# Optimization experiments

Hardware: AMD Instinct MI355X
Metric: run time of the kernel (lower is better)

The kernel has to match this reference:

```python
import jax, jax.numpy as jnp
import numpy as np

B, N, IN_DIM, HID = 16, 1024, 2, 64
GDEP = 2
ALPHA = 3.0                      # DGCRM/DGCN tanh alpha
GC_ALPHA, GC_BETA, GC_GAMMA = 0.05, 0.95, 0.95  # list_weight
HYPER, MID, NODE_DIM = 32, 16, 40
CIN = HID + IN_DIM               # 66
CAT = (GDEP + 1) * CIN           # 198


def setup_inputs() -> dict:
    key = jax.random.key(0)
    ks = jax.random.split(key, 14)
    x = jax.random.normal(ks[0], (B, N, IN_DIM), jnp.float32)
    hidden_state = 0.1 * jax.random.normal(ks[1], (B, N, HID), jnp.float32)
    nodevec1 = jax.random.normal(ks[2], (N, NODE_DIM), jnp.float32)
    nodevec2 = jax.random.normal(ks[3], (N, NODE_DIM), jnp.float32)
    A0 = jax.random.uniform(ks[4], (N, N), jnp.float32)
    A0 = A0 / A0.sum(-1, keepdims=True)
    A1 = jax.random.uniform(ks[5], (N, N), jnp.float32)
    A1 = A1 / A1.sum(-1, keepdims=True)
    s = 0.05  # small init scale
    hyper_W1 = s * jax.random.normal(ks[6], (4, CAT, HYPER), jnp.float32)
    hyper_b1 = jnp.zeros((4, HYPER), jnp.float32)
    hyper_W2 = s * jax.random.normal(ks[7], (4, HYPER, MID), jnp.float32)
    hyper_b2 = jnp.zeros((4, MID), jnp.float32)
    hyper_W3 = s * jax.random.normal(ks[8], (4, MID, NODE_DIM), jnp.float32)
    hyper_b3 = jnp.zeros((4, NODE_DIM), jnp.float32)
    rnn_W = s * jax.random.normal(ks[9], (6, CAT, HID), jnp.float32)
    rnn_b = jnp.zeros((6, HID), jnp.float32)
    return dict(x=x, hidden_state=hidden_state, nodevec1=nodevec1, nodevec2=nodevec2,
                A0=A0, A1=A1, hyper_W1=hyper_W1, hyper_b1=hyper_b1,
                hyper_W2=hyper_W2, hyper_b2=hyper_b2, hyper_W3=hyper_W3,
                hyper_b3=hyper_b3, rnn_W=rnn_W, rnn_b=rnn_b)


def reference(x, hidden_state, nodevec1, nodevec2, A0, A1,
              hyper_W1, hyper_b1, hyper_W2, hyper_b2, hyper_W3, hyper_b3,
              rnn_W, rnn_b):
    def gconv_hyper(inp, adj, i):
        # K-hop diffusion: h = alpha*x + gamma * (h^T adj) over node dim
        h = inp
        outs = [h]
        for _ in range(GDEP):
            h = GC_ALPHA * inp + GC_GAMMA * jnp.einsum('bnc,nm->bmc', h, adj)
            outs.append(h)
        ho = jnp.concatenate(outs, axis=-1)           # [B,N,(gdep+1)*CIN]
        ho = jax.nn.sigmoid(ho @ hyper_W1[i] + hyper_b1[i])
        ho = jax.nn.sigmoid(ho @ hyper_W2[i] + hyper_b2[i])
        return ho @ hyper_W3[i] + hyper_b3[i]         # [B,N,NODE_DIM]

    def gconv_rnn(inp, i):
        # FAITHFUL to source bug: stray leading '+' makes the beta/gamma
        # einsum terms standalone no-op statements, so each hop is h=alpha*x.
        outs = [inp] + [GC_ALPHA * inp] * GDEP
        return jnp.concatenate(outs, axis=-1) @ rnn_W[i] + rnn_b[i]

    # --- DGCN: dynamic adjacency generation ---
    hyper_input = jnp.concatenate((x, hidden_state), axis=-1)  # [B,N,CIN]
    filter1 = gconv_hyper(hyper_input, A0, 0) + gconv_hyper(hyper_input, A1, 1)
    filter2 = gconv_hyper(hyper_input, A0, 2) + gconv_hyper(hyper_input, A1, 3)
    nv1 = jnp.tanh(ALPHA * nodevec1[None] * filter1)  # [B,N,NODE_DIM]
    nv2 = jnp.tanh(ALPHA * nodevec2[None] * filter2)
    a = jnp.einsum('bnd,bmd->bnm', nv1, nv2) - jnp.einsum('bnd,bmd->bnm', nv2, nv1)
    adp_raw = jax.nn.relu(jnp.tanh(ALPHA * a))        # [B,N,N]
    eye = jnp.eye(N, dtype=adp_raw.dtype)
    def norm(adj):
        adj = adj + eye
        return adj / adj.sum(-1, keepdims=True)
    adp = norm(adp_raw)                               # computed as in source
    adpT = norm(jnp.swapaxes(adp_raw, 1, 2))          # (unused downstream due to
    del adp, adpT                                     #  the GConv_RNN source bug)

    # --- GRU-style gating ---
    combined = jnp.concatenate((x, hidden_state), axis=-1)
    z = jax.nn.sigmoid(gconv_rnn(combined, 0) + gconv_rnn(combined, 1))
    r = jax.nn.sigmoid(gconv_rnn(combined, 2) + gconv_rnn(combined, 3))
    candidate = jnp.concatenate((x, r * hidden_state), axis=-1)
    hc = jnp.tanh(gconv_rnn(candidate, 4) + gconv_rnn(candidate, 5))
    h = z * hidden_state + (1.0 - z) * hc             # [B,N,HID]
    return h
```

## Files before the change

### kernel.cpp

```cpp
#include <hip/hip_runtime.h>
#include <math.h>

#define NTOK   16384
#define CIN_   66
#define HID_   64
#define NCH    192
#define TPB    64

__global__ void fold_weights(const float* __restrict__ rnn_W,
                             const float* __restrict__ rnn_b,
                             float* __restrict__ Wf,
                             float* __restrict__ bf)
{
    int idx = blockIdx.x * blockDim.x + threadIdx.x;
    if (idx >= CIN_ * NCH) return;
    int k = idx / NCH;
    int c = idx - k * NCH;
    int g = c >> 6;
    int j = c & 63;
    int i0 = 2 * g, i1 = 2 * g + 1;
    const float s = 0.05f;
    float v = 0.0f;
    v += rnn_W[(i0 * 198 + k) * 64 + j]
       + s * (rnn_W[(i0 * 198 + 66 + k) * 64 + j] + rnn_W[(i0 * 198 + 132 + k) * 64 + j]);
    v += rnn_W[(i1 * 198 + k) * 64 + j]
       + s * (rnn_W[(i1 * 198 + 66 + k) * 64 + j] + rnn_W[(i1 * 198 + 132 + k) * 64 + j]);
    Wf[k * NCH + c] = v;
    if (k == 0) bf[c] = rnn_b[i0 * 64 + j] + rnn_b[i1 * 64 + j];
}

__global__ __launch_bounds__(256, 1)
void dgcrm_gru(const float* __restrict__ x,
               const float* __restrict__ h,
               const float* __restrict__ Wf,
               const float* __restrict__ bf,
               float* __restrict__ out)
{
    __shared__ float C[CIN_][TPB + 1];
    __shared__ float D[CIN_][TPB + 1];
    __shared__ float Z[HID_][TPB + 1];

    const int tid = threadIdx.x;
    const int t0  = blockIdx.x * TPB;

    {
        const float4* h4 = (const float4*)(h + (size_t)t0 * HID_);
        for (int i = tid; i < TPB * HID_ / 4; i += 256) {
            float4 v = h4[i];
            int f = i * 4;
            int t = f >> 6;
            int c = f & 63;
            C[2 + c + 0][t] = v.x;
            C[2 + c + 1][t] = v.y;
            C[2 + c + 2][t] = v.z;
            C[2 + c + 3][t] = v.w;
        }
    }
    if (tid < 2 * TPB) {
        int t = tid >> 1, k = tid & 1;
        float v = x[(size_t)(t0 + t) * 2 + k];
        C[k][t] = v;
        D[k][t] = v;
    }
    __syncthreads();

    const int wave = __builtin_amdgcn_readfirstlane(tid >> 6);
    const int lane = tid & 63;

    {
        const int ch0 = wave * 32;
        float acc[32];
        #pragma unroll
        for (int j = 0; j < 32; ++j) acc[j] = bf[ch0 + j];

        for (int k = 0; k < CIN_; ++k) {
            float ck = C[k][lane];
            const float* wrow = Wf + k * NCH + ch0;
            #pragma unroll
            for (int j = 0; j < 32; ++j) acc[j] = fmaf(ck, wrow[j], acc[j]);
        }

        if (wave < 2) {
            #pragma unroll
            for (int j = 0; j < 32; ++j) {
                float zv = 1.0f / (1.0f + __expf(-acc[j]));
                Z[ch0 + j][lane] = zv;
            }
        } else {
            const int rb = ch0 - 64;
            #pragma unroll
            for (int j = 0; j < 32; ++j) {
                float rv = 1.0f / (1.0f + __expf(-acc[j]));
                D[2 + rb + j][lane] = rv * C[2 + rb + j][lane];
            }
        }
    }
    __syncthreads();

    {
        const int ch0 = 128 + wave * 16;
        float acc[16];
        #pragma unroll
        for (int j = 0; j < 16; ++j) acc[j] = bf[ch0 + j];

        for (int k = 0; k < CIN_; ++k) {
            float ck = D[k][lane];
            const float* wrow = Wf + k * NCH + ch0;
            #pragma unroll
            for (int j = 0; j < 16; ++j) acc[j] = fmaf(ck, wrow[j], acc[j]);
        }

        const int hb = wave * 16;
        #pragma unroll
        for (int j = 0; j < 16; ++j) {
            float hc = tanhf(acc[j]);
            float zv = Z[hb + j][lane];
            float hv = C[2 + hb + j][lane];
            Z[hb + j][lane] = zv * hv + (1.0f - zv) * hc;
        }
    }
    __syncthreads();

    for (int i = tid; i < TPB * HID_; i += 256) {
        int t = i >> 6, c = i & 63;
        out[(size_t)(t0 + t) * HID_ + c] = Z[c][t];
    }
}

extern "C" void kernel_launch(void* const* d_in, const int* in_sizes, int n_in,
                              void* d_out, int out_size, void* d_ws, size_t ws_size,
                              hipStream_t stream)
{
    const float* x     = (const float*)d_in[0];
    const float* hprev = (const float*)d_in[1];
    const float* rnn_W = (const float*)d_in[12];
    const float* rnn_b = (const float*)d_in[13];

    float* Wf = (float*)d_ws;
    float* bf = Wf + CIN_ * NCH;

    fold_weights<<<(CIN_ * NCH + 255) / 256, 256, 0, stream>>>(rnn_W, rnn_b, Wf, bf);
    dgcrm_gru<<<NTOK / TPB, 256, 0, stream>>>(x, hprev, Wf, bf, (float*)d_out);
}
```

Measured before the change: 108.0 us.

## Shrink token tile to 16 and spread channels across 16-thread groups

Each block now handles 16 tokens instead of 64, so the grid grows from 256 to 1024 blocks. Inside a block, threads form 16 groups of 16 tokens, and each thread computes 8 gate channels (then 4 candidate channels) with float4 weight loads. This replaces waves that each held 32 or 16 accumulators. The output store is vectorized, tanh uses an exp-based fast form, and the launch bound no longer caps occupancy at one block. The aim is more parallelism and occupancy across the CUs, at the cost of more weight reloads per token and some LDS bank conflicts from the padded 17-wide rows.

```diff
diff --git a/kernel.cpp b/kernel.cpp
--- a/kernel.cpp
+++ b/kernel.cpp
@@ -5,7 +5,14 @@
 #define CIN_   66
 #define HID_   64
 #define NCH    192
-#define TPB    64
+#define TPB    16
+
+__device__ __forceinline__ float fast_sigmoid(float a) {
+    return 1.0f / (1.0f + __expf(-a));
+}
+__device__ __forceinline__ float fast_tanh(float a) {
+    return 1.0f - 2.0f / (__expf(2.0f * a) + 1.0f);
+}
 
 __global__ void fold_weights(const float* __restrict__ rnn_W,
                              const float* __restrict__ rnn_b,
@@ -29,7 +36,7 @@
     if (k == 0) bf[c] = rnn_b[i0 * 64 + j] + rnn_b[i1 * 64 + j];
 }
 
-__global__ __launch_bounds__(256, 1)
+__global__ __launch_bounds__(256)
 void dgcrm_gru(const float* __restrict__ x,
                const float* __restrict__ h,
                const float* __restrict__ Wf,
@@ -44,17 +51,14 @@
     const int t0  = blockIdx.x * TPB;
 
     {
-        const float4* h4 = (const float4*)(h + (size_t)t0 * HID_);
-        for (int i = tid; i < TPB * HID_ / 4; i += 256) {
-            float4 v = h4[i];
-            int f = i * 4;
-            int t = f >> 6;
-            int c = f & 63;
-            C[2 + c + 0][t] = v.x;
-            C[2 + c + 1][t] = v.y;
-            C[2 + c + 2][t] = v.z;
-            C[2 + c + 3][t] = v.w;
-        }
+        float4 v = ((const float4*)(h + (size_t)t0 * HID_))[tid];
+        int f = tid * 4;
+        int t = f >> 6;
+        int c = f & 63;
+        C[2 + c + 0][t] = v.x;
+        C[2 + c + 1][t] = v.y;
+        C[2 + c + 2][t] = v.z;
+        C[2 + c + 3][t] = v.w;
     }
     if (tid < 2 * TPB) {
         int t = tid >> 1, k = tid & 1;
@@ -64,66 +68,81 @@
     }
     __syncthreads();
 
-    const int wave = __builtin_amdgcn_readfirstlane(tid >> 6);
-    const int lane = tid & 63;
+    const int grp = tid >> 4;
+    const int tok = tid & 15;
 
     {
-        const int ch0 = wave * 32;
-        float acc[32];
-        #pragma unroll
-        for (int j = 0; j < 32; ++j) acc[j] = bf[ch0 + j];
-
+        const int ch0 = grp * 8;
+        float acc[8];
+        {
+            float4 b0 = *(const float4*)(bf + ch0);
+            float4 b1 = *(const float4*)(bf + ch0 + 4);
+            acc[0] = b0.x; acc[1] = b0.y; acc[2] = b0.z; acc[3] = b0.w;
+            acc[4] = b1.x; acc[5] = b1.y; acc[6] = b1.z; acc[7] = b1.w;
+        }
         for (int k = 0; k < CIN_; ++k) {
-            float ck = C[k][lane];
-            const float* wrow = Wf + k * NCH + ch0;
+            float ck = C[k][tok];
+            const float4* w4 = (const float4*)(Wf + k * NCH + ch0);
+            float4 w0 = w4[0];
+            float4 w1 = w4[1];
+            acc[0] = fmaf(ck, w0.x, acc[0]);
+            acc[1] = fmaf(ck, w0.y, acc[1]);
+            acc[2] = fmaf(ck, w0.z, acc[2]);
+            acc[3] = fmaf(ck, w0.w, acc[3]);
+            acc[4] = fmaf(ck, w1.x, acc[4]);
+            acc[5] = fmaf(ck, w1.y, acc[5]);
+            acc[6] = fmaf(ck, w1.z, acc[6]);
+            acc[7] = fmaf(ck, w1.w, acc[7]);
+        }
+        if (grp < 8) {
             #pragma unroll
-            for (int j = 0; j < 32; ++j) acc[j] = fmaf(ck, wrow[j], acc[j]);
-        }
-
-        if (wave < 2) {
-            #pragma unroll
-            for (int j = 0; j < 32; ++j) {
-                float zv = 1.0f / (1.0f + __expf(-acc[j]));
-                Z[ch0 + j][lane] = zv;
-            }
+            for (int j = 0; j < 8; ++j)
+                Z[ch0 + j][tok] = fast_sigmoid(acc[j]);
         } else {
             const int rb = ch0 - 64;
             #pragma unroll
-            for (int j = 0; j < 32; ++j) {
-                float rv = 1.0f / (1.0f + __expf(-acc[j]));
-                D[2 + rb + j][lane] = rv * C[2 + rb + j][lane];
-            }
+            for (int j = 0; j < 8; ++j)
+                D[2 + rb + j][tok] = fast_sigmoid(acc[j]) * C[2 + rb + j][tok];
         }
     }
     __syncthreads();
 
     {
-        const int ch0 = 128 + wave * 16;
-        float acc[16];
+        const int c0 = 128 + grp * 4;
+        float acc[4];
+        {
+            float4 b0 = *(const float4*)(bf + c0);
+            acc[0] = b0.x; acc[1] = b0.y; acc[2] = b0.z; acc[3] = b0.w;
+        }
+        for (int k = 0; k < CIN_; ++k) {
+            float dk = D[k][tok];
+            float4 w = *(const float4*)(Wf + k * NCH + c0);
+            acc[0] = fmaf(dk, w.x, acc[0]);
+            acc[1] = fmaf(dk, w.y, acc[1]);
+            acc[2] = fmaf(dk, w.z, acc[2]);
+            acc[3] = fmaf(dk, w.w, acc[3]);
+        }
+        const int hb = grp * 4;
         #pragma unroll
-        for (int j = 0; j < 16; ++j) acc[j] = bf[ch0 + j];
-
-        for (int k = 0; k < CIN_; ++k) {
-            float ck = D[k][lane];
-            const float* wrow = Wf + k * NCH + ch0;
-            #pragma unroll
-            for (int j = 0; j < 16; ++j) acc[j] = fmaf(ck, wrow[j], acc[j]);
-        }
-
-        const int hb = wave * 16;
-        #pragma unroll
-        for (int j = 0; j < 16; ++j) {
-            float hc = tanhf(acc[j]);
-            float zv = Z[hb + j][lane];
-            float hv = C[2 + hb + j][lane];
-            Z[hb + j][lane] = zv * hv + (1.0f - zv) * hc;
+        for (int j = 0; j < 4; ++j) {
+            float hc = fast_tanh(acc[j]);
+            float zv = Z[hb + j][tok];
+            float hv = C[2 + hb + j][tok];
+            Z[hb + j][tok] = zv * hv + (1.0f - zv) * hc;
         }
     }
     __syncthreads();
 
-    for (int i = tid; i < TPB * HID_; i += 256) {
-        int t = i >> 6, c = i & 63;
-        out[(size_t)(t0 + t) * HID_ + c] = Z[c][t];
+    {
+        int f = tid * 4;
+        int t = f >> 6;
+        int c = f & 63;
+        float4 r;
+        r.x = Z[c + 0][t];
+        r.y = Z[c + 1][t];
+        r.z = Z[c + 2][t];
+        r.w = Z[c + 3][t];
+        ((float4*)(out + (size_t)t0 * HID_))[tid] = r;
     }
 }
 
```

Measured after the change: 110.2 us. +2.0%, slower.
